# Performance work log

Hardware: AMD Instinct MI355X
Metric: run time of the kernel (lower is better)

## Reference

```python
import jax, jax.numpy as jnp
import numpy as np

OUT_F, IN_F, RANK, GROUP = 8192, 8192, 16, 128
N_GROUPS = OUT_F * IN_F // GROUP  # 524288
TOKENS = 256


def block_dequantize_2bit(weight_q2, weight_norm):
    """weight_q2: [n_groups, GROUP//4] int (uint8 values), weight_norm: [n_groups, 1] fp16.
    Each byte packs 4 two-bit codes little-endian (code k in bits 2k..2k+1).
    Code q in {0..3} dequantizes to ((q/3)*2 - 1) * norm."""
    shifts = jnp.array([0, 2, 4, 6], dtype=jnp.int32)
    q = (weight_q2[:, :, None] >> shifts) & 3          # [n_groups, GROUP//4, 4]
    q = q.reshape(weight_q2.shape[0], -1).astype(jnp.float32)  # [n_groups, GROUP]
    return (q * (2.0 / 3.0) - 1.0) * weight_norm.astype(jnp.float32)


def setup_inputs() -> dict:
    key = jax.random.key(0)
    ks = jax.random.split(key, 6)
    x = jax.random.normal(ks[0], (TOKENS, IN_F), dtype=jnp.float32)
    weight_q2 = jax.random.randint(ks[1], (N_GROUPS, GROUP // 4), 0, 256, dtype=jnp.int32)
    weight_norm = jax.random.uniform(ks[2], (N_GROUPS, 1), dtype=jnp.float16, minval=0.01, maxval=1.0)
    bias = jax.random.normal(ks[3], (OUT_F,), dtype=jnp.float32)
    lora_a = jax.random.normal(ks[4], (RANK, IN_F), dtype=jnp.float32) * 0.02
    lora_b = jax.random.normal(ks[5], (OUT_F, RANK), dtype=jnp.float32) * 0.02
    return {"x": x, "weight_q2": weight_q2, "weight_norm": weight_norm,
            "bias": bias, "lora_a": lora_a, "lora_b": lora_b}


def reference(x, weight_q2, weight_norm, bias, lora_a, lora_b):
    x_f32 = x.astype(jnp.float32)
    W = block_dequantize_2bit(weight_q2, weight_norm).reshape(OUT_F, IN_F)  # fp32 [out, in]
    base_out = x_f32 @ W.T + bias                       # [tokens, out]
    lora_out = (x_f32 @ lora_a.T) @ lora_b.T            # [tokens, out]
    return (base_out + lora_out).astype(x.dtype)
```

## Files before the change

kernel.cpp:

```cpp
#include <hip/hip_runtime.h>
#include <hip/hip_fp16.h>

typedef unsigned int u32;
typedef unsigned short u16;
typedef _Float16 f16x8 __attribute__((ext_vector_type(8)));
typedef float f32x4 __attribute__((ext_vector_type(4)));

#define OUT_F 8192
#define IN_F 8192
#define TOKENS 256
#define N_GROUPS 524288
#define SPLITK 4
#define KSPAN (IN_F / SPLITK)
#define KT (KSPAN / 64)

#define XB_OFF 0
#define T_OFF ((size_t)TOKENS * IN_F * 2)
#define NF_OFF (T_OFF + 65536)
#define PART_OFF (NF_OFF + (size_t)N_GROUPS * 2)
#define PART_BYTES ((size_t)SPLITK * TOKENS * OUT_F * 4)
#define WS_NEED (PART_OFF + PART_BYTES)

__device__ __forceinline__ u32 hm2(u32 a, __half2 s) {
  return __builtin_bit_cast(u32, __hmul2(__builtin_bit_cast(__half2, a), s));
}

__global__ __launch_bounds__(256) void prep(const void* __restrict__ wn,
                                            __half* __restrict__ nf,
                                            const float* __restrict__ x,
                                            const float* __restrict__ la,
                                            u16* __restrict__ xb,
                                            float* __restrict__ t) {
  int tid = threadIdx.x;
  if (blockIdx.x < 512) {
    __shared__ int votes[3];
    if (tid < 3) votes[tid] = 0;
    __syncthreads();
    const u16* pu = (const u16*)wn;
    const u32* pw = (const u32*)wn;
    int v16 = 0, vbf = 0, vf = 0;
    for (int i = tid; i < 2048; i += 256) {
      u16 u = pu[i];
      float h = __half2float(__builtin_bit_cast(__half, u));
      float b = __builtin_bit_cast(float, ((u32)u) << 16);
      if (h > 0.008f && h < 1.002f) v16++;
      if (b > 0.008f && b < 1.002f) vbf++;
    }
    for (int i = tid; i < 1024; i += 256) {
      float f = __builtin_bit_cast(float, pw[i]);
      if (f > 0.008f && f < 1.002f) vf++;
    }
    atomicAdd(&votes[0], v16);
    atomicAdd(&votes[1], vbf);
    atomicAdd(&votes[2], vf);
    __syncthreads();
    int a16 = votes[0], abf = votes[1], af32 = 2 * votes[2];
    int mode = (a16 >= abf && a16 >= af32) ? 0 : (abf >= af32 ? 1 : 2);
#pragma unroll
    for (int i = 0; i < 4; ++i) {
      int g = blockIdx.x * 1024 + i * 256 + tid;
      float v;
      if (mode == 0) v = __half2float(((const __half*)wn)[g]);
      else if (mode == 1) v = __builtin_bit_cast(float, ((u32)((const u16*)wn)[g]) << 16);
      else v = ((const float*)wn)[g];
      nf[g] = __float2half(v);
    }
    return;
  }
  int b2 = blockIdx.x - 512;
  int m = b2 & 255;
  int half = b2 >> 8;
  const float4* xr = (const float4*)(x + (size_t)m * IN_F);
  u32* xbr = (u32*)(xb + (size_t)m * IN_F);
  float pl[16];
#pragma unroll
  for (int r = 0; r < 16; ++r) pl[r] = 0.f;
#pragma unroll
  for (int it = 0; it < 4; ++it) {
    int k4 = half * 1024 + it * 256 + tid;
    float4 xv = xr[k4];
    u32 p0 = __builtin_bit_cast(u32, __float22half2_rn(make_float2(xv.x, xv.y)));
    u32 p1 = __builtin_bit_cast(u32, __float22half2_rn(make_float2(xv.z, xv.w)));
    ((uint2*)xbr)[k4] = make_uint2(p0, p1);
#pragma unroll
    for (int r = 0; r < 16; ++r) {
      const float4 av = ((const float4*)(la + (size_t)r * IN_F))[k4];
      pl[r] = fmaf(xv.x, av.x, pl[r]);
      pl[r] = fmaf(xv.y, av.y, pl[r]);
      pl[r] = fmaf(xv.z, av.z, pl[r]);
      pl[r] = fmaf(xv.w, av.w, pl[r]);
    }
  }
#pragma unroll
  for (int r = 0; r < 16; ++r) {
    float v = pl[r];
#pragma unroll
    for (int d = 32; d > 0; d >>= 1) v += __shfl_xor(v, d);
    pl[r] = v;
  }
  __shared__ float red[4][16];
  int wave = tid >> 6, lane = tid & 63;
  if (lane == 0) {
#pragma unroll
    for (int r = 0; r < 16; ++r) red[wave][r] = pl[r];
  }
  __syncthreads();
  if (tid < 16)
    t[((size_t)half * TOKENS + m) * 16 + tid] =
        red[0][tid] + red[1][tid] + red[2][tid] + red[3][tid];
}

__global__ __launch_bounds__(256) void prep2(const float* __restrict__ t,
                                             const float* __restrict__ lb,
                                             const float* __restrict__ bias,
                                             float* __restrict__ out) {
  __shared__ float tS[16 * 16];
  int tid = threadIdx.x;
  int n = blockIdx.x * 256 + tid;
  int mbase = blockIdx.y * 16;
  if (tid < 64) {
    float4 a = ((const float4*)(t + (size_t)mbase * 16))[tid];
    float4 b = ((const float4*)(t + (size_t)TOKENS * 16 + (size_t)mbase * 16))[tid];
    ((float4*)tS)[tid] = make_float4(a.x + b.x, a.y + b.y, a.z + b.z, a.w + b.w);
  }
  const float4* lbp = (const float4*)(lb + (size_t)n * 16);
  float4 b0 = lbp[0], b1 = lbp[1], b2 = lbp[2], b3 = lbp[3];
  float bv = bias[n];
  __syncthreads();
#pragma unroll
  for (int mm = 0; mm < 16; ++mm) {
    const float* tr = &tS[mm * 16];
    float a = bv;
    a += tr[0] * b0.x + tr[1] * b0.y + tr[2] * b0.z + tr[3] * b0.w;
    a += tr[4] * b1.x + tr[5] * b1.y + tr[6] * b1.z + tr[7] * b1.w;
    a += tr[8] * b2.x + tr[9] * b2.y + tr[10] * b2.z + tr[11] * b2.w;
    a += tr[12] * b3.x + tr[13] * b3.y + tr[14] * b3.z + tr[15] * b3.w;
    out[(size_t)(mbase + mm) * OUT_F + n] = a;
  }
}

__global__ __launch_bounds__(256) void finish(const float* __restrict__ t,
                                              const float* __restrict__ lb,
                                              const float* __restrict__ bias,
                                              const float* __restrict__ part,
                                              float* __restrict__ out) {
  __shared__ float tS[16 * 16];
  int tid = threadIdx.x;
  int n = blockIdx.x * 256 + tid;
  int mbase = blockIdx.y * 16;
  if (tid < 64) {
    float4 a = ((const float4*)(t + (size_t)mbase * 16))[tid];
    float4 b = ((const float4*)(t + (size_t)TOKENS * 16 + (size_t)mbase * 16))[tid];
    ((float4*)tS)[tid] = make_float4(a.x + b.x, a.y + b.y, a.z + b.z, a.w + b.w);
  }
  const float4* lbp = (const float4*)(lb + (size_t)n * 16);
  float4 b0 = lbp[0], b1 = lbp[1], b2 = lbp[2], b3 = lbp[3];
  float bv = bias[n];
  __syncthreads();
#pragma unroll
  for (int mm = 0; mm < 16; ++mm) {
    const float* tr = &tS[mm * 16];
    float a = bv;
    a += tr[0] * b0.x + tr[1] * b0.y + tr[2] * b0.z + tr[3] * b0.w;
    a += tr[4] * b1.x + tr[5] * b1.y + tr[6] * b1.z + tr[7] * b1.w;
    a += tr[8] * b2.x + tr[9] * b2.y + tr[10] * b2.z + tr[11] * b2.w;
    a += tr[12] * b3.x + tr[13] * b3.y + tr[14] * b3.z + tr[15] * b3.w;
    size_t base = (size_t)(mbase + mm) * OUT_F + n;
#pragma unroll
    for (int kz = 0; kz < SPLITK; ++kz)
      a += part[(size_t)kz * TOKENS * OUT_F + base];
    out[base] = a;
  }
}

__global__ __launch_bounds__(256, 1) void gemm_q2(const u16* __restrict__ xb,
                                                  const int* __restrict__ wq,
                                                  const __half* __restrict__ wn,
                                                  float* __restrict__ dst,
                                                  int mode) {
  __shared__ __align__(16) u16 As[128 * 64];
  __shared__ __align__(16) u16 Bs[128 * 64];
  __shared__ uint2 lut[256];

  int tid = threadIdx.x;
  int n0 = blockIdx.x * 128;
  int m0 = blockIdx.y * 128;
  int kz = blockIdx.z;
  int kbase = kz * KSPAN;

  {
    int b = tid;
    float v0 = (float)(b & 3) * (2.f / 3.f) - 1.f;
    float v1 = (float)((b >> 2) & 3) * (2.f / 3.f) - 1.f;
    float v2 = (float)((b >> 4) & 3) * (2.f / 3.f) - 1.f;
    float v3 = (float)((b >> 6) & 3) * (2.f / 3.f) - 1.f;
    u32 lo = __builtin_bit_cast(u32, __float22half2_rn(make_float2(v0, v1)));
    u32 hi = __builtin_bit_cast(u32, __float22half2_rn(make_float2(v2, v3)));
    lut[b] = make_uint2(lo, hi);
  }

  int wave = tid >> 6, lane = tid & 63;
  int quad = lane >> 4, l15 = lane & 15;
  int mo = (wave & 1) * 64, no = (wave >> 1) * 64;

  int aslot[4];
  const u16* ag[4];
#pragma unroll
  for (int i = 0; i < 4; ++i) {
    int s = tid + i * 256;
    int mm = s >> 3, c = s & 7;
    int cl = c ^ (mm & 7);
    aslot[i] = s;
    ag[i] = xb + (size_t)(m0 + mm) * IN_F + kbase + cl * 8;
  }

  int bn = tid >> 1, h = tid & 1;
  const char* gB = (const char*)wq + (size_t)(n0 + bn) * IN_F + kbase + h * 32;
  const __half* wnp = wn + (size_t)(n0 + bn) * 64 + kz * (KSPAN / 128);

  f32x4 zero4 = {0.f, 0.f, 0.f, 0.f};
  f32x4 acc[4][4];
#pragma unroll
  for (int i = 0; i < 4; ++i)
#pragma unroll
    for (int j = 0; j < 4; ++j) acc[i][j] = zero4;

  uint4 pa0, pa1, pa2, pa3;
  int4 pb0, pb1;
  __half pn;
  pa0 = *(const uint4*)(ag[0]);
  pa1 = *(const uint4*)(ag[1]);
  pa2 = *(const uint4*)(ag[2]);
  pa3 = *(const uint4*)(ag[3]);
  pb0 = *(const int4*)(gB);
  pb1 = *(const int4*)(gB + 16);
  pn = wnp[0];

#pragma unroll 1
  for (int kt = 0; kt < KT; ++kt) {
    __syncthreads();

    ((uint4*)As)[aslot[0]] = pa0;
    ((uint4*)As)[aslot[1]] = pa1;
    ((uint4*)As)[aslot[2]] = pa2;
    ((uint4*)As)[aslot[3]] = pa3;

    {
      __half2 nh = __half2half2(pn);
      int vv[8] = {pb0.x, pb0.y, pb0.z, pb0.w, pb1.x, pb1.y, pb1.z, pb1.w};
      u32 uu[16];
#pragma unroll
      for (int e = 0; e < 8; ++e) {
        uint2 lv = lut[vv[e] & 255];
        uu[2 * e] = hm2(lv.x, nh);
        uu[2 * e + 1] = hm2(lv.y, nh);
      }
      uint4* Bw = (uint4*)Bs;
#pragma unroll
      for (int cc = 0; cc < 4; ++cc) {
        int pc = (h * 4 + cc) ^ (bn & 7);
        Bw[bn * 8 + pc] = make_uint4(uu[4 * cc], uu[4 * cc + 1], uu[4 * cc + 2], uu[4 * cc + 3]);
      }
    }

    if (kt < KT - 1) {
      int ko = (kt + 1) * 64;
      pa0 = *(const uint4*)(ag[0] + ko);
      pa1 = *(const uint4*)(ag[1] + ko);
      pa2 = *(const uint4*)(ag[2] + ko);
      pa3 = *(const uint4*)(ag[3] + ko);
      pb0 = *(const int4*)(gB + ko);
      pb1 = *(const int4*)(gB + ko + 16);
      pn = wnp[(kt + 1) >> 1];
    }
    __syncthreads();

#pragma unroll
    for (int ks = 0; ks < 2; ++ks) {
      f16x8 af[4], bf[4];
#pragma unroll
      for (int mt = 0; mt < 4; ++mt) {
        int row = mo + mt * 16 + l15;
        int pc = (ks * 4 + quad) ^ (row & 7);
        af[mt] = __builtin_bit_cast(f16x8, ((const uint4*)As)[row * 8 + pc]);
      }
#pragma unroll
      for (int nt = 0; nt < 4; ++nt) {
        int row = no + nt * 16 + l15;
        int pc = (ks * 4 + quad) ^ (row & 7);
        bf[nt] = __builtin_bit_cast(f16x8, ((const uint4*)Bs)[row * 8 + pc]);
      }
#pragma unroll
      for (int mt = 0; mt < 4; ++mt)
#pragma unroll
        for (int nt = 0; nt < 4; ++nt)
          acc[mt][nt] = __builtin_amdgcn_mfma_f32_16x16x32_f16(af[mt], bf[nt], acc[mt][nt], 0, 0, 0);
    }
  }

  if (mode) {
    float* pp = dst + (size_t)kz * TOKENS * OUT_F;
#pragma unroll
    for (int mt = 0; mt < 4; ++mt)
#pragma unroll
      for (int nt = 0; nt < 4; ++nt)
#pragma unroll
        for (int r = 0; r < 4; ++r) {
          int mm = m0 + mo + mt * 16 + quad * 4 + r;
          int nn = n0 + no + nt * 16 + l15;
          pp[(size_t)mm * OUT_F + nn] = acc[mt][nt][r];
        }
  } else {
#pragma unroll
    for (int mt = 0; mt < 4; ++mt)
#pragma unroll
      for (int nt = 0; nt < 4; ++nt)
#pragma unroll
        for (int r = 0; r < 4; ++r) {
          int mm = m0 + mo + mt * 16 + quad * 4 + r;
          int nn = n0 + no + nt * 16 + l15;
          atomicAdd(&dst[(size_t)mm * OUT_F + nn], acc[mt][nt][r]);
        }
  }
}

extern "C" void kernel_launch(void* const* d_in, const int* in_sizes, int n_in,
                              void* d_out, int out_size, void* d_ws, size_t ws_size,
                              hipStream_t stream) {
  (void)in_sizes; (void)n_in; (void)out_size;
  const float* x = (const float*)d_in[0];
  const int* wq = (const int*)d_in[1];
  const void* wn_raw = d_in[2];
  const float* bias = (const float*)d_in[3];
  const float* la = (const float*)d_in[4];
  const float* lb = (const float*)d_in[5];
  float* out = (float*)d_out;

  u16* xb = (u16*)((char*)d_ws + XB_OFF);
  float* t = (float*)((char*)d_ws + T_OFF);
  __half* nf = (__half*)((char*)d_ws + NF_OFF);
  float* part = (float*)((char*)d_ws + PART_OFF);
  int usep = ws_size >= WS_NEED;

  prep<<<1024, 256, 0, stream>>>(wn_raw, nf, x, la, xb, t);
  if (usep) {
    gemm_q2<<<dim3(OUT_F / 128, TOKENS / 128, SPLITK), 256, 0, stream>>>(xb, wq, nf, part, 1);
    finish<<<dim3(OUT_F / 256, TOKENS / 16), 256, 0, stream>>>(t, lb, bias, part, out);
  } else {
    prep2<<<dim3(OUT_F / 256, TOKENS / 16), 256, 0, stream>>>(t, lb, bias, out);
    gemm_q2<<<dim3(OUT_F / 128, TOKENS / 128, SPLITK), 256, 0, stream>>>(xb, wq, nf, out, 0);
  }
}
```

Baseline: 168.4 us.

## Double-buffer A tile via direct global-to-LDS loads, raise split-K and occupancy

Activation tiles are now loaded with global_load_lds straight into a double-buffered LDS array, replacing the register round trip, so the next tile's copy overlaps the current MFMA work. Split-K goes from 4 to 8 and launch bounds allow 3 blocks per CU, to expose more parallelism and latency hiding. The trade-off is a partial-sum buffer twice as large, which adds global write and reduction traffic. It also needs more LDS per block, and the async copies must be ordered correctly by the barrier waits.

```diff
diff --git a/kernel.cpp b/kernel.cpp
--- a/kernel.cpp
+++ b/kernel.cpp
@@ -10,7 +10,7 @@
 #define IN_F 8192
 #define TOKENS 256
 #define N_GROUPS 524288
-#define SPLITK 4
+#define SPLITK 8
 #define KSPAN (IN_F / SPLITK)
 #define KT (KSPAN / 64)
 
@@ -20,6 +20,11 @@
 #define PART_OFF (NF_OFF + (size_t)N_GROUPS * 2)
 #define PART_BYTES ((size_t)SPLITK * TOKENS * OUT_F * 4)
 #define WS_NEED (PART_OFF + PART_BYTES)
+
+#define GLOAD16(g, l)                                                        \
+  __builtin_amdgcn_global_load_lds(                                          \
+      (const __attribute__((address_space(1))) void*)(g),                    \
+      (__attribute__((address_space(3))) void*)(l), 16, 0, 0)
 
 __device__ __forceinline__ u32 hm2(u32 a, __half2 s) {
   return __builtin_bit_cast(u32, __hmul2(__builtin_bit_cast(__half2, a), s));
@@ -173,12 +178,12 @@
   }
 }
 
-__global__ __launch_bounds__(256, 1) void gemm_q2(const u16* __restrict__ xb,
+__global__ __launch_bounds__(256, 3) void gemm_q2(const u16* __restrict__ xb,
                                                   const int* __restrict__ wq,
                                                   const __half* __restrict__ wn,
                                                   float* __restrict__ dst,
                                                   int mode) {
-  __shared__ __align__(16) u16 As[128 * 64];
+  __shared__ __align__(16) u16 As[2][128 * 64];
   __shared__ __align__(16) u16 Bs[128 * 64];
   __shared__ uint2 lut[256];
 
@@ -225,25 +230,16 @@
 #pragma unroll
     for (int j = 0; j < 4; ++j) acc[i][j] = zero4;
 
-  uint4 pa0, pa1, pa2, pa3;
-  int4 pb0, pb1;
-  __half pn;
-  pa0 = *(const uint4*)(ag[0]);
-  pa1 = *(const uint4*)(ag[1]);
-  pa2 = *(const uint4*)(ag[2]);
-  pa3 = *(const uint4*)(ag[3]);
-  pb0 = *(const int4*)(gB);
-  pb1 = *(const int4*)(gB + 16);
-  pn = wnp[0];
+#pragma unroll
+  for (int i = 0; i < 4; ++i) GLOAD16(ag[i], &((uint4*)As[0])[aslot[i]]);
+  int4 pb0 = *(const int4*)(gB);
+  int4 pb1 = *(const int4*)(gB + 16);
+  __half pn = wnp[0];
+  int cur = 0;
 
 #pragma unroll 1
   for (int kt = 0; kt < KT; ++kt) {
     __syncthreads();
-
-    ((uint4*)As)[aslot[0]] = pa0;
-    ((uint4*)As)[aslot[1]] = pa1;
-    ((uint4*)As)[aslot[2]] = pa2;
-    ((uint4*)As)[aslot[3]] = pa3;
 
     {
       __half2 nh = __half2half2(pn);
@@ -265,16 +261,19 @@
 
     if (kt < KT - 1) {
       int ko = (kt + 1) * 64;
-      pa0 = *(const uint4*)(ag[0] + ko);
-      pa1 = *(const uint4*)(ag[1] + ko);
-      pa2 = *(const uint4*)(ag[2] + ko);
-      pa3 = *(const uint4*)(ag[3] + ko);
+#pragma unroll
+      for (int i = 0; i < 4; ++i)
+        GLOAD16(ag[i] + ko, &((uint4*)As[cur ^ 1])[aslot[i]]);
       pb0 = *(const int4*)(gB + ko);
       pb1 = *(const int4*)(gB + ko + 16);
       pn = wnp[(kt + 1) >> 1];
     }
-    __syncthreads();
-
+
+    asm volatile("s_waitcnt lgkmcnt(0)" ::: "memory");
+    __builtin_amdgcn_s_barrier();
+    asm volatile("" ::: "memory");
+
+    const uint4* Ar = (const uint4*)As[cur];
 #pragma unroll
     for (int ks = 0; ks < 2; ++ks) {
       f16x8 af[4], bf[4];
@@ -282,7 +281,7 @@
       for (int mt = 0; mt < 4; ++mt) {
         int row = mo + mt * 16 + l15;
         int pc = (ks * 4 + quad) ^ (row & 7);
-        af[mt] = __builtin_bit_cast(f16x8, ((const uint4*)As)[row * 8 + pc]);
+        af[mt] = __builtin_bit_cast(f16x8, Ar[row * 8 + pc]);
       }
 #pragma unroll
       for (int nt = 0; nt < 4; ++nt) {
@@ -296,6 +295,7 @@
         for (int nt = 0; nt < 4; ++nt)
           acc[mt][nt] = __builtin_amdgcn_mfma_f32_16x16x32_f16(af[mt], bf[nt], acc[mt][nt], 0, 0, 0);
     }
+    cur ^= 1;
   }
 
   if (mode) {
```

After: 185.8 us. 10.3% more time.
